# Optimization experiments

Measured on AMD Instinct MI355X. Metric: run time of the kernel, lower is better.

## Reference

```python
import jax, jax.numpy as jnp
import numpy as np

EPS = 1e-08


def setup_inputs() -> dict:
    key = jax.random.key(0)
    k1, k2, k3, k4 = jax.random.split(key, 4)
    b, c, h, hw = 16, 512, 32, 32
    out_ch, kk, w_dim = 512, 3, 512
    fan_in = c * kk * kk
    return {
        "x": jax.random.normal(k1, (b, c, h, hw), dtype=jnp.float32),
        "w": jax.random.normal(k2, (b, w_dim), dtype=jnp.float32),
        "weight": jax.random.normal(k3, (out_ch, c, kk, kk), dtype=jnp.float32) / np.sqrt(fan_in),
        "affine_w": jax.random.normal(k4, (c, w_dim), dtype=jnp.float32) * 0.01,
        "affine_b": jnp.ones((c,), dtype=jnp.float32),
    }


def _modconv(x, w, weight, affine_w, affine_b, demod=True):
    b, c, h, hw = x.shape
    kk = weight.shape[-1]
    # style affine: (b, in_ch)
    style = w @ affine_w.T + affine_b
    # per-sample modulated weights: (b, out_ch, in_ch, k, k)
    wgt = weight[None] * style[:, None, :, None, None]
    if demod:
        d = jax.lax.rsqrt(jnp.sum(wgt ** 2, axis=(2, 3, 4)) + EPS)  # (b, out_ch)
        wgt = wgt * d[:, :, None, None, None]

    def conv_one(xi, wi):
        # xi: (c, h, w), wi: (out_ch, c, k, k)
        return jax.lax.conv_general_dilated(
            xi[None], wi, window_strides=(1, 1), padding="SAME",
            dimension_numbers=("NCHW", "OIHW", "NCHW"))[0]

    return jax.vmap(conv_one)(x, wgt)  # (b, out_ch, h, w)


def reference(x, w, weight, affine_w, affine_b):
    return _modconv(x, w, weight, affine_w, affine_b, demod=True)
```

## Files before the change

### kernel.cpp

```cpp
#include <hip/hip_runtime.h>


typedef __attribute__((ext_vector_type(8))) short bfx8;
typedef __attribute__((ext_vector_type(4))) float f32x4;
typedef __attribute__((ext_vector_type(4))) unsigned short us4;
typedef __attribute__((ext_vector_type(8))) unsigned short us8;

__device__ __forceinline__ unsigned short f2bf(float f) {
    unsigned int u = __builtin_bit_cast(unsigned int, f);
    u += 0x7FFFu + ((u >> 16) & 1u);
    return (unsigned short)(u >> 16);
}

__device__ __forceinline__ void gload_lds16(const void* g, void* l) {
    __builtin_amdgcn_global_load_lds(
        (const __attribute__((address_space(1))) unsigned int*)g,
        (__attribute__((address_space(3))) unsigned int*)l,
        16, 0, 0);
}

__device__ __forceinline__ float wave_sum(float v) {
    #pragma unroll
    for (int m = 1; m < 64; m <<= 1) v += __shfl_xor(v, m, 64);
    return v;
}

__device__ __forceinline__ int shift_of(int t) {
    const int tap = t >> 3, q = t & 7;
    const int ky = tap / 3, kx = tap - ky * 3;
    return (ky * 34 + kx) * 512 + q * 64;
}


__global__ void style_kernel(const float* __restrict__ w,
                             const float* __restrict__ affine_w,
                             const float* __restrict__ affine_b,
                             float* __restrict__ style) {
    const int out = blockIdx.x * 4 + (threadIdx.x >> 6);
    const int lane = threadIdx.x & 63;
    const int b = out >> 9, c = out & 511;
    const float4 a0 = *(const float4*)(affine_w + (size_t)c * 512 + lane * 8);
    const float4 a1 = *(const float4*)(affine_w + (size_t)c * 512 + lane * 8 + 4);
    const float4 w0 = *(const float4*)(w + (size_t)b * 512 + lane * 8);
    const float4 w1 = *(const float4*)(w + (size_t)b * 512 + lane * 8 + 4);
    float acc = a0.x * w0.x + a0.y * w0.y + a0.z * w0.z + a0.w * w0.w
              + a1.x * w1.x + a1.y * w1.y + a1.z * w1.z + a1.w * w1.w;
    acc = wave_sum(acc);
    if (lane == 0) style[out] = acc + affine_b[c];
}

__global__ void w2wbf_kernel(const float* __restrict__ weight,
                             float* __restrict__ W2,
                             unsigned short* __restrict__ wbf) {
    const int idx = blockIdx.x * 256 + threadIdx.x;
    const int oc = idx >> 9, c = idx & 511;
    const int q = c >> 6, c_local = c & 63;
    const int s = c_local >> 3, j = c_local & 7;
    const int pos = ((s ^ (oc & 7)) << 3) | j;
    const float* p = weight + (size_t)idx * 9;
    float ss = 0.f;
    #pragma unroll
    for (int t = 0; t < 9; ++t) {
        const float v = p[t];
        ss += v * v;
        wbf[((size_t)(t * 8 + q) * 512 + oc) * 64 + pos] = f2bf(v);
    }
    W2[idx] = ss;
}

__global__ void d_kernel(const float* __restrict__ style,
                         const float* __restrict__ W2,
                         float* __restrict__ dcoef) {
    const int out = blockIdx.x * 4 + (threadIdx.x >> 6);
    const int lane = threadIdx.x & 63;
    const int b = out >> 9, o = out & 511;
    const float4 s0 = *(const float4*)(style + (size_t)b * 512 + lane * 8);
    const float4 s1 = *(const float4*)(style + (size_t)b * 512 + lane * 8 + 4);
    const float4 v0 = *(const float4*)(W2 + (size_t)o * 512 + lane * 8);
    const float4 v1 = *(const float4*)(W2 + (size_t)o * 512 + lane * 8 + 4);
    float acc = s0.x * s0.x * v0.x + s0.y * s0.y * v0.y
              + s0.z * s0.z * v0.z + s0.w * s0.w * v0.w
              + s1.x * s1.x * v1.x + s1.y * s1.y * v1.y
              + s1.z * s1.z * v1.z + s1.w * s1.w * v1.w;
    acc = wave_sum(acc);
    if (lane == 0) dcoef[out] = rsqrtf(acc + 1e-8f);
}

__global__ void border_kernel(unsigned short* __restrict__ xs) {
    const int idx = blockIdx.x * 256 + threadIdx.x;
    const int b = idx / (132 * 128);
    const int r_ = idx - b * (132 * 128);
    const int cell = r_ >> 7, t = r_ & 127;
    int rr, cc;
    if (cell < 34)      { rr = 0;  cc = cell; }
    else if (cell < 68) { rr = 33; cc = cell - 34; }
    else { const int jj = cell - 68; rr = 1 + (jj >> 1); cc = (jj & 1) ? 33 : 0; }
    us4 z = (us4){0, 0, 0, 0};
    *(us4*)(xs + (((size_t)b * 34 + rr) * 34 + cc) * 512 + t * 4) = z;
}

__global__ void xspad_kernel(const float* __restrict__ x,
                             const float* __restrict__ style,
                             unsigned short* __restrict__ xs) {
    __shared__ __align__(16) unsigned short tile[128][36];
    const int b = blockIdx.z, h = blockIdx.y, c0 = blockIdx.x * 128;
    const int tid = threadIdx.x;
    #pragma unroll
    for (int it = 0; it < 4; ++it) {
        const int e = it * 256 + tid;
        const int ch = e >> 3, w4 = e & 7;
        const float4 v = *(const float4*)(x + (((size_t)b * 512 + c0 + ch) * 32 + h) * 32 + w4 * 4);
        const float sv = style[b * 512 + c0 + ch];
        us4 o;
        o.x = f2bf(v.x * sv); o.y = f2bf(v.y * sv);
        o.z = f2bf(v.z * sv); o.w = f2bf(v.w * sv);
        *(us4*)&tile[ch][w4 * 4] = o;
    }
    __syncthreads();
    #pragma unroll
    for (int it = 0; it < 2; ++it) {
        const int e = it * 256 + tid;
        const int cq = e & 15, w_ = e >> 4;
        us8 o;
        #pragma unroll
        for (int i = 0; i < 8; ++i) o[i] = tile[cq * 8 + i][w_];
        *(us8*)(xs + (((size_t)b * 34 + (h + 1)) * 34 + (w_ + 1)) * 512 + c0 + cq * 8) = o;
    }
}

#define LDS_RD(off) (*(const bfx8*)(lds + (off)))
#define MFMA(a, bb, c) __builtin_amdgcn_mfma_f32_16x16x32_bf16((a), (bb), (c), 0, 0, 0)

__global__ __launch_bounds__(512, 2) void conv_kernel(
    const unsigned short* __restrict__ wbf,
    const unsigned short* __restrict__ xs,
    const float* __restrict__ dcoef,
    float* __restrict__ out) {
    __shared__ __align__(16) char lds[147456];

    const int id = blockIdx.x;
    const int wid = (id & 7) * 32 + (id >> 3);
    const int b = wid >> 4;
    const int oc0 = ((wid >> 2) & 3) << 7;
    const int n0  = (wid & 3) << 8;

    const int tid = threadIdx.x;
    const int lane = tid & 63;
    const int wv = tid >> 6;
    const int wr = wv >> 2, wc = wv & 3;
    const int l7 = lane & 7, l15 = lane & 15;

    const int swz0 = ((lane >> 4) ^ l7) << 4;
    const int swz1 = (((lane >> 4) + 4) ^ l7) << 4;
    const int arow = (wr * 64 + l15) * 128;
    const int brow = 16384 + (wc * 64 + l15) * 128;

    const int lsub = lane >> 3;
    const int sx = l7 ^ lsub;
    const int ra0 = wv * 16 + lsub, ra1 = ra0 + 8;
    const int aoff0 = (oc0 + ra0) * 64 + l7 * 8;
    const int aoff1 = (oc0 + ra1) * 64 + l7 * 8;
    const int adst0 = (wv * 2) * 1024, adst1 = adst0 + 1024;
    size_t bbase[4]; int bdst[4];
    const size_t xsb = (size_t)b * (34 * 34 * 512);
    #pragma unroll
    for (int i = 0; i < 4; ++i) {
        const int p = wv * 32 + i * 8 + lsub;
        const int n = n0 + p;
        bbase[i] = xsb + ((size_t)(n >> 5) * 34 + (n & 31)) * 512 + sx * 8;
        bdst[i] = 16384 + (wv * 4 + i) * 1024;
    }

#define STAGE_A(tt, bo) do { \
        const unsigned short* wsrc_ = wbf + (size_t)(tt) * 32768; \
        gload_lds16(wsrc_ + aoff0, lds + (bo) + adst0); \
        gload_lds16(wsrc_ + aoff1, lds + (bo) + adst1); } while (0)
#define STAGE_B01(sh, bo) do { \
        gload_lds16(xs + bbase[0] + (sh), lds + (bo) + bdst[0]); \
        gload_lds16(xs + bbase[1] + (sh), lds + (bo) + bdst[1]); } while (0)
#define STAGE_B23(sh, bo) do { \
        gload_lds16(xs + bbase[2] + (sh), lds + (bo) + bdst[2]); \
        gload_lds16(xs + bbase[3] + (sh), lds + (bo) + bdst[3]); } while (0)
#define BARRIER() __builtin_amdgcn_s_barrier()

    f32x4 acc[4][4];
    #pragma unroll
    for (int i = 0; i < 4; ++i)
        #pragma unroll
        for (int j = 0; j < 4; ++j) acc[i][j] = (f32x4){0.f, 0.f, 0.f, 0.f};

    STAGE_A(0, 0);      STAGE_B01(0, 0);       STAGE_B23(0, 0);
    STAGE_A(1, 49152);  STAGE_B01(64, 49152);  STAGE_B23(64, 49152);
    asm volatile("s_waitcnt vmcnt(6)" ::: "memory");
    BARRIER();

    int co = 0;
    for (int t = 0; t < 72; ++t) {
        int so = co + 98304; if (so >= 147456) so -= 147456;
        const bool pf = (t < 70);
        const int sh2 = pf ? shift_of(t + 2) : 0;

        bfx8 af0[4], bf0[4], af1[4], bf1[4];

        #pragma unroll
        for (int mi = 0; mi < 4; ++mi) af0[mi] = LDS_RD(co + arow + mi * 2048 + swz0);
        #pragma unroll
        for (int ni = 0; ni < 4; ++ni) bf0[ni] = LDS_RD(co + brow + ni * 2048 + swz0);
        #pragma unroll
        for (int mi = 0; mi < 4; ++mi) af1[mi] = LDS_RD(co + arow + mi * 2048 + swz1);
        #pragma unroll
        for (int ni = 0; ni < 4; ++ni) bf1[ni] = LDS_RD(co + brow + ni * 2048 + swz1);

        if (pf) { STAGE_A(t + 2, so); STAGE_B01(sh2, so); STAGE_B23(sh2, so); }

        __builtin_amdgcn_s_setprio(1);
        #pragma unroll
        for (int ni = 0; ni < 4; ++ni)
            #pragma unroll
            for (int mi = 0; mi < 4; ++mi)
                acc[mi][ni] = MFMA(af0[mi], bf0[ni], acc[mi][ni]);
        #pragma unroll
        for (int ni = 0; ni < 4; ++ni)
            #pragma unroll
            for (int mi = 0; mi < 4; ++mi)
                acc[mi][ni] = MFMA(af1[mi], bf1[ni], acc[mi][ni]);
        __builtin_amdgcn_s_setprio(0);

        if (t < 70) { asm volatile("s_waitcnt vmcnt(6)" ::: "memory"); }
        else        { asm volatile("s_waitcnt vmcnt(0)" ::: "memory"); }
        BARRIER();

        co += 49152; if (co >= 147456) co -= 147456;
    }

    const int r4 = (lane >> 4) * 4;
    #pragma unroll
    for (int mi = 0; mi < 4; ++mi) {
        #pragma unroll
        for (int rr = 0; rr < 4; ++rr) {
            const int ocr = oc0 + wr * 64 + mi * 16 + r4 + rr;
            const float dv = dcoef[b * 512 + ocr];
            float* orow = out + ((size_t)b * 512 + ocr) * 1024 + n0 + wc * 64 + l15;
            #pragma unroll
            for (int ni = 0; ni < 4; ++ni)
                orow[ni * 16] = acc[mi][ni][rr] * dv;
        }
    }
}

extern "C" void kernel_launch(void* const* d_in, const int* in_sizes, int n_in,
                              void* d_out, int out_size, void* d_ws, size_t ws_size,
                              hipStream_t stream) {
    const float* x        = (const float*)d_in[0];
    const float* w        = (const float*)d_in[1];
    const float* weight   = (const float*)d_in[2];
    const float* affine_w = (const float*)d_in[3];
    const float* affine_b = (const float*)d_in[4];
    float* out = (float*)d_out;

    char* ws = (char*)d_ws;
    float*          style = (float*)(ws + 0);
    float*          W2    = (float*)(ws + 0x8000);
    float*          dcoef = (float*)(ws + 0x108000);
    unsigned short* wbf   = (unsigned short*)(ws + 0x110000);
    unsigned short* xs    = (unsigned short*)(ws + 0x590000);

    style_kernel<<<2048, 256, 0, stream>>>(w, affine_w, affine_b, style);
    w2wbf_kernel<<<1024, 256, 0, stream>>>(weight, W2, wbf);
    d_kernel<<<2048, 256, 0, stream>>>(style, W2, dcoef);
    border_kernel<<<1056, 256, 0, stream>>>(xs);
    xspad_kernel<<<dim3(4, 32, 16), 256, 0, stream>>>(x, style, xs);
    conv_kernel<<<256, 512, 0, stream>>>(wbf, xs, dcoef, out);
}
```

Baseline: 98.32 us.

## Load weight operand directly from global into registers, stage only activations in LDS

Result: slower. 135.9 us (+38.3%).

```diff
diff --git a/kernel.cpp b/kernel.cpp
--- a/kernel.cpp
+++ b/kernel.cpp
@@ -136,7 +136,7 @@
     const unsigned short* __restrict__ xs,
     const float* __restrict__ dcoef,
     float* __restrict__ out) {
-    __shared__ __align__(16) char lds[147456];
+    __shared__ __align__(16) char lds[98304];
 
     const int id = blockIdx.x;
     const int wid = (id & 7) * 32 + (id >> 3);
@@ -152,15 +152,19 @@
 
     const int swz0 = ((lane >> 4) ^ l7) << 4;
     const int swz1 = (((lane >> 4) + 4) ^ l7) << 4;
-    const int arow = (wr * 64 + l15) * 128;
-    const int brow = 16384 + (wc * 64 + l15) * 128;
+    const int brow = (wc * 64 + l15) * 128;
+
+    const char* wbf8 = (const char*)wbf;
+    int aofs0[4], aofs1[4];
+    #pragma unroll
+    for (int mi = 0; mi < 4; ++mi) {
+        const int row = oc0 + wr * 64 + mi * 16 + l15;
+        aofs0[mi] = row * 128 + (((lane >> 4)    ) ^ l7) * 16;
+        aofs1[mi] = row * 128 + (((lane >> 4) + 4) ^ l7) * 16;
+    }
 
     const int lsub = lane >> 3;
     const int sx = l7 ^ lsub;
-    const int ra0 = wv * 16 + lsub, ra1 = ra0 + 8;
-    const int aoff0 = (oc0 + ra0) * 64 + l7 * 8;
-    const int aoff1 = (oc0 + ra1) * 64 + l7 * 8;
-    const int adst0 = (wv * 2) * 1024, adst1 = adst0 + 1024;
     size_t bbase[4]; int bdst[4];
     const size_t xsb = (size_t)b * (34 * 34 * 512);
     #pragma unroll
@@ -168,17 +172,12 @@
         const int p = wv * 32 + i * 8 + lsub;
         const int n = n0 + p;
         bbase[i] = xsb + ((size_t)(n >> 5) * 34 + (n & 31)) * 512 + sx * 8;
-        bdst[i] = 16384 + (wv * 4 + i) * 1024;
-    }
-
-#define STAGE_A(tt, bo) do { \
-        const unsigned short* wsrc_ = wbf + (size_t)(tt) * 32768; \
-        gload_lds16(wsrc_ + aoff0, lds + (bo) + adst0); \
-        gload_lds16(wsrc_ + aoff1, lds + (bo) + adst1); } while (0)
-#define STAGE_B01(sh, bo) do { \
+        bdst[i] = (wv * 4 + i) * 1024;
+    }
+
+#define STAGE_B(sh, bo) do { \
         gload_lds16(xs + bbase[0] + (sh), lds + (bo) + bdst[0]); \
-        gload_lds16(xs + bbase[1] + (sh), lds + (bo) + bdst[1]); } while (0)
-#define STAGE_B23(sh, bo) do { \
+        gload_lds16(xs + bbase[1] + (sh), lds + (bo) + bdst[1]); \
         gload_lds16(xs + bbase[2] + (sh), lds + (bo) + bdst[2]); \
         gload_lds16(xs + bbase[3] + (sh), lds + (bo) + bdst[3]); } while (0)
 #define BARRIER() __builtin_amdgcn_s_barrier()
@@ -189,29 +188,31 @@
         #pragma unroll
         for (int j = 0; j < 4; ++j) acc[i][j] = (f32x4){0.f, 0.f, 0.f, 0.f};
 
-    STAGE_A(0, 0);      STAGE_B01(0, 0);       STAGE_B23(0, 0);
-    STAGE_A(1, 49152);  STAGE_B01(64, 49152);  STAGE_B23(64, 49152);
-    asm volatile("s_waitcnt vmcnt(6)" ::: "memory");
+    STAGE_B(0, 0);
+    STAGE_B(64, 32768);
+    asm volatile("s_waitcnt vmcnt(4)" ::: "memory");
     BARRIER();
 
     int co = 0;
     for (int t = 0; t < 72; ++t) {
-        int so = co + 98304; if (so >= 147456) so -= 147456;
+        int so = co + 65536; if (so >= 98304) so -= 98304;
         const bool pf = (t < 70);
         const int sh2 = pf ? shift_of(t + 2) : 0;
 
-        bfx8 af0[4], bf0[4], af1[4], bf1[4];
-
-        #pragma unroll
-        for (int mi = 0; mi < 4; ++mi) af0[mi] = LDS_RD(co + arow + mi * 2048 + swz0);
+        bfx8 af0[4], af1[4], bf0[4], bf1[4];
+
         #pragma unroll
         for (int ni = 0; ni < 4; ++ni) bf0[ni] = LDS_RD(co + brow + ni * 2048 + swz0);
         #pragma unroll
-        for (int mi = 0; mi < 4; ++mi) af1[mi] = LDS_RD(co + arow + mi * 2048 + swz1);
-        #pragma unroll
         for (int ni = 0; ni < 4; ++ni) bf1[ni] = LDS_RD(co + brow + ni * 2048 + swz1);
 
-        if (pf) { STAGE_A(t + 2, so); STAGE_B01(sh2, so); STAGE_B23(sh2, so); }
+        const char* ap = wbf8 + (size_t)t * 65536;
+        #pragma unroll
+        for (int mi = 0; mi < 4; ++mi) af0[mi] = *(const bfx8*)(ap + aofs0[mi]);
+        #pragma unroll
+        for (int mi = 0; mi < 4; ++mi) af1[mi] = *(const bfx8*)(ap + aofs1[mi]);
+
+        if (pf) STAGE_B(sh2, so);
 
         __builtin_amdgcn_s_setprio(1);
         #pragma unroll
@@ -226,11 +227,8 @@
                 acc[mi][ni] = MFMA(af1[mi], bf1[ni], acc[mi][ni]);
         __builtin_amdgcn_s_setprio(0);
 
-        if (t < 70) { asm volatile("s_waitcnt vmcnt(6)" ::: "memory"); }
-        else        { asm volatile("s_waitcnt vmcnt(0)" ::: "memory"); }
         BARRIER();
-
-        co += 49152; if (co >= 147456) co -= 147456;
+        co += 32768; if (co >= 98304) co -= 98304;
     }
 
     const int r4 = (lane >> 4) * 4;
```

## Use 4 waves per block with 128x64 per-wave tiles in conv kernel

Applied to the files above, without the earlier changes.

After: 105.5 us. 7.3% more time.

```diff
diff --git a/kernel.cpp b/kernel.cpp
--- a/kernel.cpp
+++ b/kernel.cpp
@@ -131,7 +131,7 @@
 #define LDS_RD(off) (*(const bfx8*)(lds + (off)))
 #define MFMA(a, bb, c) __builtin_amdgcn_mfma_f32_16x16x32_bf16((a), (bb), (c), 0, 0, 0)
 
-__global__ __launch_bounds__(512, 2) void conv_kernel(
+__global__ __launch_bounds__(256, 1) void conv_kernel(
     const unsigned short* __restrict__ wbf,
     const unsigned short* __restrict__ xs,
     const float* __restrict__ dcoef,
@@ -147,87 +147,89 @@
     const int tid = threadIdx.x;
     const int lane = tid & 63;
     const int wv = tid >> 6;
-    const int wr = wv >> 2, wc = wv & 3;
     const int l7 = lane & 7, l15 = lane & 15;
 
     const int swz0 = ((lane >> 4) ^ l7) << 4;
     const int swz1 = (((lane >> 4) + 4) ^ l7) << 4;
-    const int arow = (wr * 64 + l15) * 128;
-    const int brow = 16384 + (wc * 64 + l15) * 128;
+    const int arow = l15 * 128;
+    const int brow = 16384 + (wv * 64 + l15) * 128;
 
     const int lsub = lane >> 3;
     const int sx = l7 ^ lsub;
-    const int ra0 = wv * 16 + lsub, ra1 = ra0 + 8;
-    const int aoff0 = (oc0 + ra0) * 64 + l7 * 8;
-    const int aoff1 = (oc0 + ra1) * 64 + l7 * 8;
-    const int adst0 = (wv * 2) * 1024, adst1 = adst0 + 1024;
-    size_t bbase[4]; int bdst[4];
+    int aoff[4];
+    #pragma unroll
+    for (int i = 0; i < 4; ++i) {
+        const int ra = (wv * 4 + i) * 8 + lsub;
+        aoff[i] = (oc0 + ra) * 64 + l7 * 8;
+    }
+    const int adst = (wv * 4) * 1024;
+    size_t bbase[8];
     const size_t xsb = (size_t)b * (34 * 34 * 512);
     #pragma unroll
-    for (int i = 0; i < 4; ++i) {
-        const int p = wv * 32 + i * 8 + lsub;
+    for (int i = 0; i < 8; ++i) {
+        const int p = wv * 64 + i * 8 + lsub;
         const int n = n0 + p;
         bbase[i] = xsb + ((size_t)(n >> 5) * 34 + (n & 31)) * 512 + sx * 8;
-        bdst[i] = 16384 + (wv * 4 + i) * 1024;
-    }
-
-#define STAGE_A(tt, bo) do { \
+    }
+    const int bdst = 16384 + (wv * 8) * 1024;
+
+#define STAGE_ALL(tt, bo) do { \
         const unsigned short* wsrc_ = wbf + (size_t)(tt) * 32768; \
-        gload_lds16(wsrc_ + aoff0, lds + (bo) + adst0); \
-        gload_lds16(wsrc_ + aoff1, lds + (bo) + adst1); } while (0)
-#define STAGE_B01(sh, bo) do { \
-        gload_lds16(xs + bbase[0] + (sh), lds + (bo) + bdst[0]); \
-        gload_lds16(xs + bbase[1] + (sh), lds + (bo) + bdst[1]); } while (0)
-#define STAGE_B23(sh, bo) do { \
-        gload_lds16(xs + bbase[2] + (sh), lds + (bo) + bdst[2]); \
-        gload_lds16(xs + bbase[3] + (sh), lds + (bo) + bdst[3]); } while (0)
+        const int sh_ = shift_of(tt); \
+        _Pragma("unroll") \
+        for (int i_ = 0; i_ < 4; ++i_) \
+            gload_lds16(wsrc_ + aoff[i_], lds + (bo) + adst + i_ * 1024); \
+        _Pragma("unroll") \
+        for (int i_ = 0; i_ < 8; ++i_) \
+            gload_lds16(xs + bbase[i_] + sh_, lds + (bo) + bdst + i_ * 1024); } while (0)
+
 #define BARRIER() __builtin_amdgcn_s_barrier()
 
-    f32x4 acc[4][4];
-    #pragma unroll
-    for (int i = 0; i < 4; ++i)
+    f32x4 acc[8][4];
+    #pragma unroll
+    for (int i = 0; i < 8; ++i)
         #pragma unroll
         for (int j = 0; j < 4; ++j) acc[i][j] = (f32x4){0.f, 0.f, 0.f, 0.f};
 
-    STAGE_A(0, 0);      STAGE_B01(0, 0);       STAGE_B23(0, 0);
-    STAGE_A(1, 49152);  STAGE_B01(64, 49152);  STAGE_B23(64, 49152);
-    asm volatile("s_waitcnt vmcnt(6)" ::: "memory");
+    STAGE_ALL(0, 0);
+    STAGE_ALL(1, 49152);
+    asm volatile("s_waitcnt vmcnt(12)" ::: "memory");
     BARRIER();
 
     int co = 0;
+    #pragma unroll 1
     for (int t = 0; t < 72; ++t) {
         int so = co + 98304; if (so >= 147456) so -= 147456;
         const bool pf = (t < 70);
-        const int sh2 = pf ? shift_of(t + 2) : 0;
-
-        bfx8 af0[4], bf0[4], af1[4], bf1[4];
-
-        #pragma unroll
-        for (int mi = 0; mi < 4; ++mi) af0[mi] = LDS_RD(co + arow + mi * 2048 + swz0);
+
+        bfx8 af0[8], bf0[4], af1[8], bf1[4];
+
+        #pragma unroll
+        for (int mi = 0; mi < 8; ++mi) af0[mi] = LDS_RD(co + arow + mi * 2048 + swz0);
         #pragma unroll
         for (int ni = 0; ni < 4; ++ni) bf0[ni] = LDS_RD(co + brow + ni * 2048 + swz0);
         #pragma unroll
-        for (int mi = 0; mi < 4; ++mi) af1[mi] = LDS_RD(co + arow + mi * 2048 + swz1);
+        for (int mi = 0; mi < 8; ++mi) af1[mi] = LDS_RD(co + arow + mi * 2048 + swz1);
         #pragma unroll
         for (int ni = 0; ni < 4; ++ni) bf1[ni] = LDS_RD(co + brow + ni * 2048 + swz1);
 
-        if (pf) { STAGE_A(t + 2, so); STAGE_B01(sh2, so); STAGE_B23(sh2, so); }
+        if (pf) STAGE_ALL(t + 2, so);
 
         __builtin_amdgcn_s_setprio(1);
         #pragma unroll
         for (int ni = 0; ni < 4; ++ni)
             #pragma unroll
-            for (int mi = 0; mi < 4; ++mi)
+            for (int mi = 0; mi < 8; ++mi)
                 acc[mi][ni] = MFMA(af0[mi], bf0[ni], acc[mi][ni]);
         #pragma unroll
         for (int ni = 0; ni < 4; ++ni)
             #pragma unroll
-            for (int mi = 0; mi < 4; ++mi)
+            for (int mi = 0; mi < 8; ++mi)
                 acc[mi][ni] = MFMA(af1[mi], bf1[ni], acc[mi][ni]);
         __builtin_amdgcn_s_setprio(0);
 
-        if (t < 70) { asm volatile("s_waitcnt vmcnt(6)" ::: "memory"); }
-        else        { asm volatile("s_waitcnt vmcnt(0)" ::: "memory"); }
+        if (t < 70) { asm volatile("s_waitcnt vmcnt(12)" ::: "memory"); }
+        else        { asm volatile("s_waitcnt vmcnt(0)"  ::: "memory"); }
         BARRIER();
 
         co += 49152; if (co >= 147456) co -= 147456;
@@ -235,12 +237,12 @@
 
     const int r4 = (lane >> 4) * 4;
     #pragma unroll
-    for (int mi = 0; mi < 4; ++mi) {
+    for (int mi = 0; mi < 8; ++mi) {
         #pragma unroll
         for (int rr = 0; rr < 4; ++rr) {
-            const int ocr = oc0 + wr * 64 + mi * 16 + r4 + rr;
+            const int ocr = oc0 + mi * 16 + r4 + rr;
             const float dv = dcoef[b * 512 + ocr];
-            float* orow = out + ((size_t)b * 512 + ocr) * 1024 + n0 + wc * 64 + l15;
+            float* orow = out + ((size_t)b * 512 + ocr) * 1024 + n0 + wv * 64 + l15;
             #pragma unroll
             for (int ni = 0; ni < 4; ++ni)
                 orow[ni * 16] = acc[mi][ni][rr] * dv;
@@ -270,5 +272,5 @@
     d_kernel<<<2048, 256, 0, stream>>>(style, W2, dcoef);
     border_kernel<<<1056, 256, 0, stream>>>(xs);
     xspad_kernel<<<dim3(4, 32, 16), 256, 0, stream>>>(x, style, xs);
-    conv_kernel<<<256, 512, 0, stream>>>(wbf, xs, dcoef, out);
-}
+    conv_kernel<<<256, 256, 0, stream>>>(wbf, xs, dcoef, out);
+}
```
